# Performance work log

Hardware: AMD Instinct MI355X
Metric: run time of the kernel (lower is better)

Reference implementation:

```python
import jax, jax.numpy as jnp
import numpy as np

B = 64
N_SNPS = 500000
N_GENES = 20000
N_NODES = 600000
N_FILTERS = 8
EPS = 1e-5  # torch BatchNorm1d default


def setup_inputs() -> dict:
    key = jax.random.key(0)
    ks = jax.random.split(key, 14)
    snp = jax.random.normal(ks[0], (B, N_SNPS), dtype=jnp.float32)
    snp_ids = jax.random.randint(ks[1], (N_NODES,), 0, N_SNPS, dtype=jnp.int32)
    node_gene = jax.random.randint(ks[2], (N_NODES,), 0, N_GENES, dtype=jnp.int32)
    # learned params
    filters = jax.random.normal(ks[3], (N_FILTERS, N_SNPS), dtype=jnp.float32) * 0.001
    W1 = jax.random.normal(ks[4], (N_GENES, 1024), dtype=jnp.float32) * 0.02
    b1 = jnp.zeros((1024,), jnp.float32)
    g1 = 1.0 + 0.02 * jax.random.normal(ks[5], (1024,), dtype=jnp.float32)
    beta1 = jnp.zeros((1024,), jnp.float32)
    W2 = jax.random.normal(ks[6], (1024, 256), dtype=jnp.float32) * 0.02
    b2 = jnp.zeros((256,), jnp.float32)
    g2 = 1.0 + 0.02 * jax.random.normal(ks[7], (256,), dtype=jnp.float32)
    beta2 = jnp.zeros((256,), jnp.float32)
    W3 = jax.random.normal(ks[8], (256, 1), dtype=jnp.float32) * 0.02
    b3 = jnp.zeros((1,), jnp.float32)
    return {"snp": snp, "snp_ids": snp_ids, "node_gene": node_gene,
            "filters": filters, "W1": W1, "b1": b1, "g1": g1, "beta1": beta1,
            "W2": W2, "b2": b2, "g2": g2, "beta2": beta2, "W3": W3, "b3": b3}


def _batchnorm(x, gamma, beta):
    # training-mode batch statistics over the batch axis (biased var)
    m = jnp.mean(x, axis=0)
    v = jnp.var(x, axis=0)
    return gamma * (x - m) * jax.lax.rsqrt(v + EPS) + beta


def reference(snp, snp_ids, node_gene, filters, W1, b1, g1, beta1,
              W2, b2, g2, beta2, W3, b3):
    # Original: snp_h[b,n,f] = snp[b,n]*filters[f,n]; per-sample gather by snp_ids,
    # DGL sum-readout per gene, then mean over filter channel. Since readout-sum
    # and channel-mean are linear, fuse: per-SNP weight = mean_f filters[f,:].
    w = jnp.mean(filters, axis=0)                      # [n_snps]
    node = snp[:, snp_ids] * w[snp_ids][None, :]       # [B, n_nodes]
    gene = jnp.zeros((snp.shape[0], N_GENES), snp.dtype)
    gene = gene.at[:, node_gene].add(node)             # batched segment-sum -> [B, n_genes]
    # predictor MLP (dropout = identity in eval; BN uses batch stats)
    h = jax.nn.relu(_batchnorm(gene @ W1 + b1, g1, beta1))
    h = jax.nn.relu(_batchnorm(h @ W2 + b2, g2, beta2))
    preds = h @ W3 + b3                                # [B, 1]
    return preds, filters
```

## Files before the change

### kernel.cpp

```cpp
#include <hip/hip_runtime.h>

#define NS 500000
#define NG 20000
#define NN 600000
#define NF 8
#define EPS_ 1e-5f

__global__ __launch_bounds__(256) void k_w_copy(const float* __restrict__ filters,
                                                float* __restrict__ w,
                                                float* __restrict__ out_f) {
  int i = blockIdx.x * 256 + threadIdx.x;
  const int n4 = NS / 4;
  if (i >= n4) return;
  const float4* f4 = (const float4*)filters;
  float4* o4 = (float4*)out_f;
  float sx = 0.f, sy = 0.f, sz = 0.f, sw = 0.f;
#pragma unroll
  for (int f = 0; f < NF; f++) {
    float4 v = f4[(size_t)f * n4 + i];
    o4[(size_t)f * n4 + i] = v;
    sx += v.x; sy += v.y; sz += v.z; sw += v.w;
  }
  float4 r;
  r.x = sx * 0.125f; r.y = sy * 0.125f; r.z = sz * 0.125f; r.w = sw * 0.125f;
  ((float4*)w)[i] = r;
}

__global__ __launch_bounds__(256) void k_hist_mark(const int* __restrict__ snp_ids,
                                                   const int* __restrict__ node_gene,
                                                   int* __restrict__ cnt,
                                                   unsigned char* __restrict__ used) {
  int j = blockIdx.x * 256 + threadIdx.x;
  if (j < NN) {
    used[snp_ids[j]] = 1;
    atomicAdd(&cnt[node_gene[j]], 1);
  }
}

__global__ __launch_bounds__(1024) void k_scan(const int* __restrict__ cnt,
                                               int* __restrict__ offs,
                                               int* __restrict__ cursor) {
  __shared__ int part[1024];
  int t = threadIdx.x;
  int base = t * 20;
  int s = 0;
  for (int i = 0; i < 20; i++) {
    int g = base + i;
    if (g < NG) s += cnt[g];
  }
  part[t] = s;
  __syncthreads();
  for (int d = 1; d < 1024; d <<= 1) {
    int v = 0;
    if (t >= d) v = part[t - d];
    __syncthreads();
    part[t] += v;
    __syncthreads();
  }
  int run = part[t] - s;
  for (int i = 0; i < 20; i++) {
    int g = base + i;
    if (g < NG) {
      offs[g] = run;
      cursor[g] = run;
      run += cnt[g];
    }
  }
  if (t == 1023) offs[NG] = part[1023];
}

__global__ __launch_bounds__(256) void k_sortnodes(const int* __restrict__ snp_ids,
                                                   const int* __restrict__ node_gene,
                                                   int* __restrict__ cursor,
                                                   int* __restrict__ sorted_sid) {
  int j = blockIdx.x * 256 + threadIdx.x;
  if (j >= NN) return;
  int g = node_gene[j];
  int pos = atomicAdd(&cursor[g], 1);
  sorted_sid[pos] = snp_ids[j];
}

__global__ __launch_bounds__(256) void k_transpose(const float* __restrict__ snp,
                                                   const float* __restrict__ w,
                                                   const unsigned char* __restrict__ used,
                                                   float* __restrict__ snpT) {
  __shared__ float tile[64 * 64];
  int t = threadIdx.x;
  int s0 = blockIdx.x * 64;

  int f = t & 15;
  int r = (t >> 4) & 3;
  int wq = t >> 6;
  bool okf = (s0 + 4 * f + 4 <= NS);
  float4 w4 = make_float4(0.f, 0.f, 0.f, 0.f);
  if (okf) w4 = *(const float4*)(w + s0 + 4 * f);
  float4 v[4];
#pragma unroll
  for (int i = 0; i < 4; i++) {
    int b = wq * 16 + i * 4 + r;
    v[i] = make_float4(0.f, 0.f, 0.f, 0.f);
    if (okf) v[i] = *(const float4*)(snp + (size_t)b * NS + s0 + 4 * f);
  }
#pragma unroll
  for (int i = 0; i < 4; i++) {
    int b = wq * 16 + i * 4 + r;
    float4 x = v[i];
    x.x *= w4.x; x.y *= w4.y; x.z *= w4.z; x.w *= w4.w;
    ((float4*)tile)[b * 16 + (f ^ (b & 15))] = x;
  }
  __syncthreads();

  int b = t & 63;
  int sq = t >> 6;
  int ubase = s0 + sq * 16;
  unsigned u32s[4];
  if (ubase + 16 <= NS) {
    uint4 ub = *(const uint4*)(used + ubase);
    u32s[0] = ub.x; u32s[1] = ub.y; u32s[2] = ub.z; u32s[3] = ub.w;
  } else {
#pragma unroll
    for (int i = 0; i < 4; i++) {
      unsigned vv = 0;
#pragma unroll
      for (int k = 0; k < 4; k++) {
        int s = ubase + 4 * i + k;
        if (s < NS && used[s]) vv |= (1u << (8 * k));
      }
      u32s[i] = vv;
    }
  }
#pragma unroll
  for (int i = 0; i < 4; i++) {
    int s4 = sq * 4 + i;
    float4 x = ((const float4*)tile)[b * 16 + (s4 ^ (b & 15))];
    int sb = s0 + 4 * s4;
    float xv[4] = {x.x, x.y, x.z, x.w};
#pragma unroll
    for (int k = 0; k < 4; k++) {
      int s = sb + k;
      bool u = ((u32s[i] >> (8 * k)) & 0xFFu) != 0;
      if (s < NS && u) snpT[(size_t)s * 64 + b] = xv[k];
    }
  }
}

__global__ __launch_bounds__(256) void k_accum_T(const float* __restrict__ snpT,
                                                 const int* __restrict__ offs,
                                                 const int* __restrict__ sorted_sid,
                                                 float* __restrict__ geneT) {
  int wave = (blockIdx.x * 256 + threadIdx.x) >> 6;
  int lane = threadIdx.x & 63;
  if (wave >= NG) return;
  int beg = offs[wave], end = offs[wave + 1];
  float a0 = 0.f, a1 = 0.f, a2 = 0.f, a3 = 0.f;
  int n = beg;
  for (; n + 8 <= end; n += 8) {
    int i0 = sorted_sid[n + 0];
    int i1 = sorted_sid[n + 1];
    int i2 = sorted_sid[n + 2];
    int i3 = sorted_sid[n + 3];
    int i4 = sorted_sid[n + 4];
    int i5 = sorted_sid[n + 5];
    int i6 = sorted_sid[n + 6];
    int i7 = sorted_sid[n + 7];
    float v0 = snpT[(size_t)i0 * 64 + lane];
    float v1 = snpT[(size_t)i1 * 64 + lane];
    float v2 = snpT[(size_t)i2 * 64 + lane];
    float v3 = snpT[(size_t)i3 * 64 + lane];
    float v4 = snpT[(size_t)i4 * 64 + lane];
    float v5 = snpT[(size_t)i5 * 64 + lane];
    float v6 = snpT[(size_t)i6 * 64 + lane];
    float v7 = snpT[(size_t)i7 * 64 + lane];
    a0 += v0; a1 += v1; a2 += v2; a3 += v3;
    a0 += v4; a1 += v5; a2 += v6; a3 += v7;
  }
  for (; n + 4 <= end; n += 4) {
    int i0 = sorted_sid[n + 0];
    int i1 = sorted_sid[n + 1];
    int i2 = sorted_sid[n + 2];
    int i3 = sorted_sid[n + 3];
    a0 += snpT[(size_t)i0 * 64 + lane];
    a1 += snpT[(size_t)i1 * 64 + lane];
    a2 += snpT[(size_t)i2 * 64 + lane];
    a3 += snpT[(size_t)i3 * 64 + lane];
  }
  for (; n < end; n++) a0 += snpT[(size_t)sorted_sid[n] * 64 + lane];
  geneT[(size_t)wave * 64 + lane] = (a0 + a1) + (a2 + a3);
}

template <int KPSMAX>
__global__ __launch_bounds__(256) void k_gemm_stream2(const float* __restrict__ XT,
                                                      const float* __restrict__ Wm,
                                                      float* __restrict__ partial,
                                                      int KTOT, int kPerSlice,
                                                      int NCOLS) {
  __shared__ float xs[KPSMAX * 64];
  int tid = threadIdx.x;
  int lane = tid & 63;
  int wv = tid >> 6;
  int c0 = blockIdx.x * 128 + lane * 2;
  int b0 = wv * 16;
  int nslice = gridDim.y;
  int kBeg = blockIdx.y * kPerSlice;
  int kEnd = KTOT < kBeg + kPerSlice ? KTOT : kBeg + kPerSlice;
  int kc = kEnd - kBeg;

  {
    const float4* src = (const float4*)(XT + (size_t)kBeg * 64);
    float4* dst = (float4*)xs;
    for (int i = tid; i < kc * 16; i += 256) dst[i] = src[i];
  }
  __syncthreads();

  float acc0[16], acc1[16];
#pragma unroll
  for (int j = 0; j < 16; j++) { acc0[j] = 0.f; acc1[j] = 0.f; }

  const float* wp = Wm + (size_t)kBeg * NCOLS + c0;
  float2 w0 = make_float2(0.f, 0.f);
  float2 w1 = make_float2(0.f, 0.f);
  if (kc > 0) w0 = *(const float2*)(wp);
  if (kc > 1) w1 = *(const float2*)(wp + NCOLS);

  int kk = 0;
#pragma unroll 2
  for (; kk + 2 < kc; kk++) {
    float2 wn = *(const float2*)(wp + (size_t)(kk + 2) * NCOLS);
    const float4* xp = (const float4*)(xs + kk * 64 + b0);
    float4 g0 = xp[0], g1 = xp[1], g2 = xp[2], g3 = xp[3];
    float gg[16];
    gg[0] = g0.x; gg[1] = g0.y; gg[2] = g0.z; gg[3] = g0.w;
    gg[4] = g1.x; gg[5] = g1.y; gg[6] = g1.z; gg[7] = g1.w;
    gg[8] = g2.x; gg[9] = g2.y; gg[10] = g2.z; gg[11] = g2.w;
    gg[12] = g3.x; gg[13] = g3.y; gg[14] = g3.z; gg[15] = g3.w;
#pragma unroll
    for (int j = 0; j < 16; j++) {
      acc0[j] = fmaf(w0.x, gg[j], acc0[j]);
      acc1[j] = fmaf(w0.y, gg[j], acc1[j]);
    }
    w0 = w1; w1 = wn;
  }
  for (; kk < kc; kk++) {
    const float4* xp = (const float4*)(xs + kk * 64 + b0);
    float4 g0 = xp[0], g1 = xp[1], g2 = xp[2], g3 = xp[3];
    float gg[16];
    gg[0] = g0.x; gg[1] = g0.y; gg[2] = g0.z; gg[3] = g0.w;
    gg[4] = g1.x; gg[5] = g1.y; gg[6] = g1.z; gg[7] = g1.w;
    gg[8] = g2.x; gg[9] = g2.y; gg[10] = g2.z; gg[11] = g2.w;
    gg[12] = g3.x; gg[13] = g3.y; gg[14] = g3.z; gg[15] = g3.w;
#pragma unroll
    for (int j = 0; j < 16; j++) {
      acc0[j] = fmaf(w0.x, gg[j], acc0[j]);
      acc1[j] = fmaf(w0.y, gg[j], acc1[j]);
    }
    w0 = w1;
  }

#pragma unroll
  for (int i = 0; i < 2; i++) {
    const float* a = (i == 0) ? acc0 : acc1;
    float4* dst = (float4*)(partial + ((size_t)(c0 + i) * nslice + blockIdx.y) * 64 + b0);
#pragma unroll
    for (int q = 0; q < 4; q++) {
      float4 vv;
      vv.x = a[q * 4 + 0]; vv.y = a[q * 4 + 1];
      vv.z = a[q * 4 + 2]; vv.w = a[q * 4 + 3];
      dst[q] = vv;
    }
  }
}

__global__ __launch_bounds__(256) void k_reduce_bn(const float* __restrict__ partial,
                                                   int S,
                                                   const float* __restrict__ gamma,
                                                   const float* __restrict__ beta,
                                                   float* __restrict__ outT) {
  int n = blockIdx.x * 4 + (threadIdx.x >> 6);
  int b = threadIdx.x & 63;
  const float* p = partial + (size_t)n * S * 64 + b;
  float x0 = 0.f, x1 = 0.f, x2 = 0.f, x3 = 0.f;
  float x4 = 0.f, x5 = 0.f, x6 = 0.f, x7 = 0.f;
  int s = 0;
  for (; s + 8 <= S; s += 8) {
    x0 += p[(s + 0) * 64];
    x1 += p[(s + 1) * 64];
    x2 += p[(s + 2) * 64];
    x3 += p[(s + 3) * 64];
    x4 += p[(s + 4) * 64];
    x5 += p[(s + 5) * 64];
    x6 += p[(s + 6) * 64];
    x7 += p[(s + 7) * 64];
  }
  for (; s < S; s++) x0 += p[s * 64];
  float x = ((x0 + x1) + (x2 + x3)) + ((x4 + x5) + (x6 + x7));
  float s1 = x, s2 = x * x;
#pragma unroll
  for (int d = 32; d > 0; d >>= 1) {
    s1 += __shfl_xor(s1, d, 64);
    s2 += __shfl_xor(s2, d, 64);
  }
  float m = s1 * (1.f / 64.f);
  float v = s2 * (1.f / 64.f) - m * m;
  float y = gamma[n] * (x - m) * rsqrtf(v + EPS_) + beta[n];
  outT[(size_t)n * 64 + b] = fmaxf(y, 0.f);
}

__global__ __launch_bounds__(64) void k_head(const float* __restrict__ h2T,
                                             const float* __restrict__ W3,
                                             const float* __restrict__ b3,
                                             float* __restrict__ out) {
  int b = threadIdx.x;
  float acc = 0.f;
  for (int k = 0; k < 256; k++) acc = fmaf(h2T[(size_t)k * 64 + b], W3[k], acc);
  out[b] = acc + b3[0];
}

static constexpr int S1 = 125;
static constexpr int S2 = 64;
static constexpr size_t N_W = NS;
static constexpr size_t N_SNPT = (size_t)NS * 64;
static constexpr size_t N_GENET = (size_t)NG * 64;
static constexpr size_t N_P1 = (size_t)S1 * 1024 * 64;
static constexpr size_t N_P2 = (size_t)S2 * 256 * 64;

extern "C" void kernel_launch(void* const* d_in, const int* in_sizes, int n_in,
                              void* d_out, int out_size, void* d_ws, size_t ws_size,
                              hipStream_t stream) {
  const float* snp       = (const float*)d_in[0];
  const int*   snp_ids   = (const int*)d_in[1];
  const int*   node_gene = (const int*)d_in[2];
  const float* filters   = (const float*)d_in[3];
  const float* W1        = (const float*)d_in[4];
  const float* g1        = (const float*)d_in[6];
  const float* beta1     = (const float*)d_in[7];
  const float* W2        = (const float*)d_in[8];
  const float* g2        = (const float*)d_in[10];
  const float* beta2     = (const float*)d_in[11];
  const float* W3        = (const float*)d_in[12];
  const float* b3        = (const float*)d_in[13];
  float* out = (float*)d_out;
  float* ws  = (float*)d_ws;

  float* w      = ws;
  float* snpT   = ws + N_W;
  float* p1     = snpT;
  float* p2     = p1 + N_P1;
  float* geneT  = snpT + N_SNPT;
  float* h1T    = geneT + N_GENET;
  float* h2T    = h1T + 65536;
  int* cnt      = (int*)(h2T + 16384);
  int* offs     = cnt + NG;
  int* cursor   = offs + 20064;
  int* sorted   = cursor + NG;
  unsigned char* used = (unsigned char*)(sorted + NN);

  hipMemsetAsync(cnt, 0, NG * sizeof(int), stream);
  hipMemsetAsync(used, 0, NS, stream);

  k_w_copy<<<(NS / 4 + 255) / 256, 256, 0, stream>>>(filters, w, out + 64);

  k_hist_mark<<<(NN + 255) / 256, 256, 0, stream>>>(snp_ids, node_gene, cnt, used);
  k_scan<<<1, 1024, 0, stream>>>(cnt, offs, cursor);
  k_sortnodes<<<(NN + 255) / 256, 256, 0, stream>>>(snp_ids, node_gene, cursor, sorted);

  k_transpose<<<(NS + 63) / 64, 256, 0, stream>>>(snp, w, used, snpT);
  k_accum_T<<<(NG * 64) / 256, 256, 0, stream>>>(snpT, offs, sorted, geneT);

  k_gemm_stream2<160><<<dim3(8, S1), 256, 0, stream>>>(geneT, W1, p1, NG, 160, 1024);
  k_reduce_bn<<<1024 / 4, 256, 0, stream>>>(p1, S1, g1, beta1, h1T);

  k_gemm_stream2<16><<<dim3(2, S2), 256, 0, stream>>>(h1T, W2, p2, 1024, 16, 256);
  k_reduce_bn<<<256 / 4, 256, 0, stream>>>(p2, S2, g2, beta2, h2T);

  k_head<<<1, 64, 0, stream>>>(h2T, W3, b3, out);
}
```

Baseline: 486.5 us.

## Double-buffer transpose tiles so each block prefetches the next tile while storing

The transpose kernel now has each block process four consecutive 64-SNP tiles using two shared-memory buffers. Loads of the next tile's snp, weight and used-mask are issued before the current tile is written out, so global reads overlap with the scattered snpT stores. This cuts the grid to a quarter of the blocks and doubles shared memory per block. Both changes can reduce occupancy and the latency hiding that came from many independent blocks.

```diff
diff --git a/kernel.cpp b/kernel.cpp
--- a/kernel.cpp
+++ b/kernel.cpp
@@ -84,63 +84,122 @@
                                                    const float* __restrict__ w,
                                                    const unsigned char* __restrict__ used,
                                                    float* __restrict__ snpT) {
-  __shared__ float tile[64 * 64];
+  __shared__ float tile[2][64 * 64];
+  const int NT = (NS + 63) / 64;
   int t = threadIdx.x;
-  int s0 = blockIdx.x * 64;
-
   int f = t & 15;
   int r = (t >> 4) & 3;
   int wq = t >> 6;
-  bool okf = (s0 + 4 * f + 4 <= NS);
-  float4 w4 = make_float4(0.f, 0.f, 0.f, 0.f);
-  if (okf) w4 = *(const float4*)(w + s0 + 4 * f);
-  float4 v[4];
-#pragma unroll
-  for (int i = 0; i < 4; i++) {
-    int b = wq * 16 + i * 4 + r;
-    v[i] = make_float4(0.f, 0.f, 0.f, 0.f);
-    if (okf) v[i] = *(const float4*)(snp + (size_t)b * NS + s0 + 4 * f);
-  }
-#pragma unroll
-  for (int i = 0; i < 4; i++) {
-    int b = wq * 16 + i * 4 + r;
-    float4 x = v[i];
-    x.x *= w4.x; x.y *= w4.y; x.z *= w4.z; x.w *= w4.w;
-    ((float4*)tile)[b * 16 + (f ^ (b & 15))] = x;
-  }
-  __syncthreads();
-
   int b = t & 63;
   int sq = t >> 6;
-  int ubase = s0 + sq * 16;
-  unsigned u32s[4];
-  if (ubase + 16 <= NS) {
-    uint4 ub = *(const uint4*)(used + ubase);
-    u32s[0] = ub.x; u32s[1] = ub.y; u32s[2] = ub.z; u32s[3] = ub.w;
-  } else {
+
+  int t0 = blockIdx.x * 4;
+  if (t0 >= NT) return;
+
+  float4 cw;
+  float4 cv[4];
+  unsigned cu32[4];
+
+  {
+    int s0 = t0 * 64;
+    bool okf = (s0 + 4 * f + 4 <= NS);
+    cw = make_float4(0.f, 0.f, 0.f, 0.f);
+    if (okf) cw = *(const float4*)(w + s0 + 4 * f);
 #pragma unroll
     for (int i = 0; i < 4; i++) {
-      unsigned vv = 0;
-#pragma unroll
-      for (int k = 0; k < 4; k++) {
-        int s = ubase + 4 * i + k;
-        if (s < NS && used[s]) vv |= (1u << (8 * k));
+      int bb = wq * 16 + i * 4 + r;
+      cv[i] = make_float4(0.f, 0.f, 0.f, 0.f);
+      if (okf) cv[i] = *(const float4*)(snp + (size_t)bb * NS + s0 + 4 * f);
+    }
+    int ubase = s0 + sq * 16;
+    if (ubase + 16 <= NS) {
+      uint4 ub = *(const uint4*)(used + ubase);
+      cu32[0] = ub.x; cu32[1] = ub.y; cu32[2] = ub.z; cu32[3] = ub.w;
+    } else {
+#pragma unroll
+      for (int i = 0; i < 4; i++) {
+        unsigned vv = 0;
+#pragma unroll
+        for (int kk = 0; kk < 4; kk++) {
+          int s = ubase + 4 * i + kk;
+          if (s < NS && used[s]) vv |= (1u << (8 * kk));
+        }
+        cu32[i] = vv;
       }
-      u32s[i] = vv;
-    }
-  }
-#pragma unroll
-  for (int i = 0; i < 4; i++) {
-    int s4 = sq * 4 + i;
-    float4 x = ((const float4*)tile)[b * 16 + (s4 ^ (b & 15))];
-    int sb = s0 + 4 * s4;
-    float xv[4] = {x.x, x.y, x.z, x.w};
-#pragma unroll
-    for (int k = 0; k < 4; k++) {
-      int s = sb + k;
-      bool u = ((u32s[i] >> (8 * k)) & 0xFFu) != 0;
-      if (s < NS && u) snpT[(size_t)s * 64 + b] = xv[k];
-    }
+    }
+#pragma unroll
+    for (int i = 0; i < 4; i++) {
+      int bb = wq * 16 + i * 4 + r;
+      float4 x = cv[i];
+      x.x *= cw.x; x.y *= cw.y; x.z *= cw.z; x.w *= cw.w;
+      ((float4*)tile[0])[bb * 16 + (f ^ (bb & 15))] = x;
+    }
+  }
+  __syncthreads();
+
+  for (int k = 0; k < 4; k++) {
+    int tt = t0 + k;
+    if (tt >= NT) break;
+    int cur = k & 1;
+    bool hasNext = (k + 1 < 4) && (tt + 1 < NT);
+
+    float4 nw = make_float4(0.f, 0.f, 0.f, 0.f);
+    float4 nv[4];
+    unsigned nu32[4];
+    if (hasNext) {
+      int s0 = (tt + 1) * 64;
+      bool okf = (s0 + 4 * f + 4 <= NS);
+      if (okf) nw = *(const float4*)(w + s0 + 4 * f);
+#pragma unroll
+      for (int i = 0; i < 4; i++) {
+        int bb = wq * 16 + i * 4 + r;
+        nv[i] = make_float4(0.f, 0.f, 0.f, 0.f);
+        if (okf) nv[i] = *(const float4*)(snp + (size_t)bb * NS + s0 + 4 * f);
+      }
+      int ubase = s0 + sq * 16;
+      if (ubase + 16 <= NS) {
+        uint4 ub = *(const uint4*)(used + ubase);
+        nu32[0] = ub.x; nu32[1] = ub.y; nu32[2] = ub.z; nu32[3] = ub.w;
+      } else {
+#pragma unroll
+        for (int i = 0; i < 4; i++) {
+          unsigned vv = 0;
+#pragma unroll
+          for (int kk = 0; kk < 4; kk++) {
+            int s = ubase + 4 * i + kk;
+            if (s < NS && used[s]) vv |= (1u << (8 * kk));
+          }
+          nu32[i] = vv;
+        }
+      }
+    }
+
+    int s0c = tt * 64;
+#pragma unroll
+    for (int i = 0; i < 4; i++) {
+      int s4 = sq * 4 + i;
+      float4 x = ((const float4*)tile[cur])[b * 16 + (s4 ^ (b & 15))];
+      int sb = s0c + 4 * s4;
+      float xv[4] = {x.x, x.y, x.z, x.w};
+#pragma unroll
+      for (int kk = 0; kk < 4; kk++) {
+        int s = sb + kk;
+        bool u = ((cu32[i] >> (8 * kk)) & 0xFFu) != 0;
+        if (s < NS && u) snpT[(size_t)s * 64 + b] = xv[kk];
+      }
+    }
+
+    if (hasNext) {
+#pragma unroll
+      for (int i = 0; i < 4; i++) {
+        int bb = wq * 16 + i * 4 + r;
+        float4 x = nv[i];
+        x.x *= nw.x; x.y *= nw.y; x.z *= nw.z; x.w *= nw.w;
+        ((float4*)tile[cur ^ 1])[bb * 16 + (f ^ (bb & 15))] = x;
+      }
+      cu32[0] = nu32[0]; cu32[1] = nu32[1]; cu32[2] = nu32[2]; cu32[3] = nu32[3];
+    }
+    __syncthreads();
   }
 }
 
@@ -363,7 +422,11 @@
   k_scan<<<1, 1024, 0, stream>>>(cnt, offs, cursor);
   k_sortnodes<<<(NN + 255) / 256, 256, 0, stream>>>(snp_ids, node_gene, cursor, sorted);
 
-  k_transpose<<<(NS + 63) / 64, 256, 0, stream>>>(snp, w, used, snpT);
+  {
+    int nt = (NS + 63) / 64;
+    int nb = (nt + 3) / 4;
+    k_transpose<<<nb, 256, 0, stream>>>(snp, w, used, snpT);
+  }
   k_accum_T<<<(NG * 64) / 256, 256, 0, stream>>>(snpT, offs, sorted, geneT);
 
   k_gemm_stream2<160><<<dim3(8, S1), 256, 0, stream>>>(geneT, W1, p1, NG, 160, 1024);
```

Result: no change. 488.6 us (+0.4%).
